# Kernel optimization log

Hardware: AMD Instinct MI355X
Metric: run time of the kernel (lower is better)

Reference implementation:

```python
import jax, jax.numpy as jnp
import numpy as np

MAX_N = 32        # mixture degree N
N_PTS = 16384     # number of scalar inputs
INIT_DECAY = 1.0


def setup_inputs() -> dict:
    key = jax.random.key(0)
    k1, _ = jax.random.split(key)
    # inputs assumed elementwise in [-1, 1]
    xs = jax.random.uniform(k1, (N_PTS,), dtype=jnp.float32, minval=-1.0, maxval=1.0)
    # learned logits param, init logits[n] = -n * init_decay (as in __init__)
    logits = -INIT_DECAY * jnp.arange(MAX_N + 1, dtype=jnp.float32)
    return {"xs": xs, "logits": logits}


def _psi(xs, logits, max_n):
    """psi(x) = concat_n sqrt(w_n) * phi_n(x); shape (P, 2*max_n+1).

    phi_0 = [1]; phi_n = [T_n(x), sqrt(1-x^2) * U_{n-1}(x)] for n>=1.
    Single linear-pass recurrence instead of per-degree recompute.
    """
    w = jax.nn.softmax(logits)          # (max_n+1,)
    sw = jnp.sqrt(w)
    xc = jnp.clip(xs, -1.0, 1.0)        # (P,)
    s = jnp.sqrt(jnp.clip(1.0 - xc * xc, 0.0))
    P = xs.shape[0]

    # T_0..T_max_n and U_0..U_max_n via one shared recurrence (fixed small loop)
    Ts = [jnp.ones_like(xc), xc]
    Us = [jnp.ones_like(xc), 2.0 * xc]
    for _ in range(2, max_n + 1):
        Ts.append(2.0 * xc * Ts[-1] - Ts[-2])
        Us.append(2.0 * xc * Us[-1] - Us[-2])
    T = jnp.stack(Ts, axis=-1)          # (P, max_n+1)
    U = jnp.stack(Us, axis=-1)          # (P, max_n+1)

    Tn = T[:, 1:]                       # T_1..T_N            (P, max_n)
    Un = U[:, :max_n]                   # U_0..U_{N-1}        (P, max_n)
    # interleave per degree: [T_n, s * U_{n-1}], weighted by sqrt(w_n)
    pair = jnp.stack([Tn, s[:, None] * Un], axis=-1)   # (P, max_n, 2)
    pair = pair * sw[1:][None, :, None]
    head = sw[0] * jnp.ones((P, 1), dtype=xs.dtype)    # sqrt(w_0) * phi_0
    return jnp.concatenate([head, pair.reshape(P, 2 * max_n)], axis=-1)


def reference(xs, logits):
    """gram(xs) = psi(xs) @ psi(xs)^T, shape (P, P)."""
    psi = _psi(xs, logits, MAX_N)       # (P, 2*MAX_N+1)
    return psi @ psi.T
```

## Files before the change

### kernel.cpp

```cpp
#include <hip/hip_runtime.h>
#include <hip/hip_bf16.h>
#include <math.h>

#define MAXN    32
#define NPTS    16384
#define RSTRIDE 64
#define BTA     64
#define BTB     128
#define NCHUNK  ((BTA + BTB) * RSTRIDE * 2 / 1024)
#define W0_OFF  (NPTS * RSTRIDE)

typedef __attribute__((ext_vector_type(8))) short         bf16x8;
typedef __attribute__((ext_vector_type(4))) float         f32x4;
typedef __attribute__((ext_vector_type(4))) unsigned int  u32x4;

__device__ inline ushort f2bf(float f) {
    union { float f; unsigned u; } v; v.f = f;
    unsigned u = v.u;
    u += 0x7FFFu + ((u >> 16) & 1u);
    return (ushort)(u >> 16);
}

__global__ __launch_bounds__(256) void psi_kernel(
    const float* __restrict__ xs, const float* __restrict__ logits,
    ushort* __restrict__ psi, float* __restrict__ w0scr)
{
    int pt = blockIdx.x * blockDim.x + threadIdx.x;
    if (pt >= NPTS) return;

    float x = xs[pt];
    x = fminf(1.0f, fmaxf(-1.0f, x));
    float s = sqrtf(fmaxf(0.0f, 1.0f - x * x));

    float m = -3.4e38f;
    #pragma unroll
    for (int n = 0; n <= MAXN; ++n) m = fmaxf(m, logits[n]);
    float sum = 0.0f;
    #pragma unroll
    for (int n = 0; n <= MAXN; ++n) sum += __expf(logits[n] - m);
    float inv = 1.0f / sum;

    if (pt == 0) w0scr[0] = __expf(logits[0] - m) * inv;

    ushort tmp[RSTRIDE];
    float Tm1 = 1.0f, T = x;
    float Um1 = 1.0f, U = 2.0f * x;
    float tx = 2.0f * x;
    #pragma unroll
    for (int n = 1; n <= MAXN; ++n) {
        float swn = sqrtf(__expf(logits[n] - m) * inv);
        tmp[2 * n - 2] = f2bf(swn * T);
        tmp[2 * n - 1] = f2bf(swn * (s * Um1));
        float Tn = tx * T - Tm1; Tm1 = T; T = Tn;
        float Un = tx * U - Um1; Um1 = U; U = Un;
    }

    u32x4* dst = (u32x4*)(psi + (size_t)pt * RSTRIDE);
    const u32x4* src = (const u32x4*)tmp;
    const int rx = pt & 7;
    #pragma unroll
    for (int j = 0; j < 8; ++j) dst[j ^ rx] = src[j];
}

__device__ inline void load_lds16(const void* g, void* l) {
    __builtin_amdgcn_global_load_lds(
        (const __attribute__((address_space(1))) unsigned*)g,
        (__attribute__((address_space(3))) unsigned*)l, 16, 0, 0);
}

__global__ __launch_bounds__(256, 5) void gram_kernel(
    const ushort* __restrict__ psi, const float* __restrict__ w0scr,
    float* __restrict__ out)
{
    __shared__ float ldsF[BTA * BTB];

    const int tid  = threadIdx.x;
    const int w    = tid >> 6;
    const int lane = tid & 63;
    const int bi   = blockIdx.y;
    const int bj   = blockIdx.x;

    const float w0 = w0scr[0];

    {
        const char* gA = (const char*)(psi + (size_t)bi * BTA * RSTRIDE);
        const char* gB = (const char*)(psi + (size_t)bj * BTB * RSTRIDE);
        char* lbase = (char*)ldsF;
        for (int q = w; q < NCHUNK; q += 4) {
            const char* src = (q < 8) ? (gA + q * 1024) : (gB + (q - 8) * 1024);
            load_lds16(src + lane * 16, lbase + q * 1024);
        }
    }
    __syncthreads();

    const int lr = lane & 15;
    const int lh = lane >> 4;
    const int cq = lh * 4;

    const char* aRow   = (const char*)ldsF + (w * 16 + lr) * 128;
    const char* bPanel = (const char*)ldsF + 8192;

    f32x4 acc[8];
    #pragma unroll
    for (int ct = 0; ct < 8; ++ct) acc[ct] = (f32x4){w0, w0, w0, w0};

    #pragma unroll
    for (int ks = 0; ks < 2; ++ks) {
        const int slot = (ks * 4 + lh);
        bf16x8 a = *(const bf16x8*)(aRow + ((slot ^ (lr & 7)) * 16));
        #pragma unroll
        for (int ct = 0; ct < 8; ++ct) {
            const char* bRow = bPanel + (ct * 16 + lr) * 128;
            bf16x8 b = *(const bf16x8*)(bRow + ((slot ^ (lr & 7)) * 16));
            acc[ct] = __builtin_amdgcn_mfma_f32_16x16x32_bf16(b, a, acc[ct], 0, 0, 0);
        }
    }

    __syncthreads();
    {
        const int row = w * 16 + lr;
        const int rxe = (row & 7) << 2;
        #pragma unroll
        for (int ct = 0; ct < 8; ++ct) {
            int col = (cq + ct * 16) ^ rxe;
            *(f32x4*)(ldsF + row * BTB + col) = acc[ct];
        }
    }
    __syncthreads();

    {
        const int rsub = tid >> 5;
        const int col  = (tid & 31) * 4;
        #pragma unroll
        for (int p = 0; p < 8; ++p) {
            int row  = p * 8 + rsub;
            int colr = col ^ ((row & 7) << 2);
            f32x4 v = *(const f32x4*)(ldsF + row * BTB + colr);
            float* dst = out + (size_t)(bi * BTA + row) * NPTS + (size_t)bj * BTB + col;
            *(f32x4*)dst = v;
        }
    }
}

extern "C" void kernel_launch(void* const* d_in, const int* in_sizes, int n_in,
                              void* d_out, int out_size, void* d_ws, size_t ws_size,
                              hipStream_t stream) {
    const float* xs     = (const float*)d_in[0];
    const float* logits = (const float*)d_in[1];
    float* out          = (float*)d_out;
    ushort* psi         = (ushort*)d_ws;
    float*  w0scr       = (float*)((char*)d_ws + (size_t)W0_OFF * 2);

    psi_kernel<<<NPTS / 256, 256, 0, stream>>>(xs, logits, psi, w0scr);

    dim3 grid(NPTS / BTB, NPTS / BTA);
    gram_kernel<<<grid, 256, 0, stream>>>(psi, w0scr, out);
}
```

Before: 200.4 us.

## Widen gram tile to 64x256, stage psi rows through LDS for coalesced stores

```diff
diff --git a/kernel.cpp b/kernel.cpp
--- a/kernel.cpp
+++ b/kernel.cpp
@@ -6,7 +6,7 @@
 #define NPTS    16384
 #define RSTRIDE 64
 #define BTA     64
-#define BTB     128
+#define BTB     256
 #define NCHUNK  ((BTA + BTB) * RSTRIDE * 2 / 1024)
 #define W0_OFF  (NPTS * RSTRIDE)
 
@@ -25,8 +25,10 @@
     const float* __restrict__ xs, const float* __restrict__ logits,
     ushort* __restrict__ psi, float* __restrict__ w0scr)
 {
-    int pt = blockIdx.x * blockDim.x + threadIdx.x;
-    if (pt >= NPTS) return;
+    __shared__ ushort srow[256 * RSTRIDE];
+
+    const int tid = threadIdx.x;
+    const int pt  = blockIdx.x * 256 + tid;
 
     float x = xs[pt];
     x = fminf(1.0f, fmaxf(-1.0f, x));
@@ -55,11 +57,21 @@
         float Un = tx * U - Um1; Um1 = U; U = Un;
     }
 
-    u32x4* dst = (u32x4*)(psi + (size_t)pt * RSTRIDE);
-    const u32x4* src = (const u32x4*)tmp;
-    const int rx = pt & 7;
-    #pragma unroll
-    for (int j = 0; j < 8; ++j) dst[j ^ rx] = src[j];
+    {
+        u32x4* lrow = (u32x4*)(srow + tid * RSTRIDE);
+        const u32x4* src = (const u32x4*)tmp;
+        const int rx = tid & 7;
+        #pragma unroll
+        for (int j = 0; j < 8; ++j) lrow[j ^ rx] = src[j];
+    }
+    __syncthreads();
+
+    {
+        const u32x4* ls = (const u32x4*)srow;
+        u32x4* gd = (u32x4*)(psi + (size_t)blockIdx.x * 256 * RSTRIDE);
+        #pragma unroll
+        for (int i = 0; i < 8; ++i) gd[i * 256 + tid] = ls[i * 256 + tid];
+    }
 }
 
 __device__ inline void load_lds16(const void* g, void* l) {
@@ -68,7 +80,7 @@
         (__attribute__((address_space(3))) unsigned*)l, 16, 0, 0);
 }
 
-__global__ __launch_bounds__(256, 5) void gram_kernel(
+__global__ __launch_bounds__(256) void gram_kernel(
     const ushort* __restrict__ psi, const float* __restrict__ w0scr,
     float* __restrict__ out)
 {
@@ -100,18 +112,17 @@
     const char* aRow   = (const char*)ldsF + (w * 16 + lr) * 128;
     const char* bPanel = (const char*)ldsF + 8192;
 
-    f32x4 acc[8];
+    f32x4 acc[16];
     #pragma unroll
-    for (int ct = 0; ct < 8; ++ct) acc[ct] = (f32x4){w0, w0, w0, w0};
+    for (int ct = 0; ct < 16; ++ct) acc[ct] = (f32x4){w0, w0, w0, w0};
 
     #pragma unroll
     for (int ks = 0; ks < 2; ++ks) {
-        const int slot = (ks * 4 + lh);
-        bf16x8 a = *(const bf16x8*)(aRow + ((slot ^ (lr & 7)) * 16));
+        const int sx = ((ks * 4 + lh) ^ (lr & 7)) * 16;
+        bf16x8 a = *(const bf16x8*)(aRow + sx);
         #pragma unroll
-        for (int ct = 0; ct < 8; ++ct) {
-            const char* bRow = bPanel + (ct * 16 + lr) * 128;
-            bf16x8 b = *(const bf16x8*)(bRow + ((slot ^ (lr & 7)) * 16));
+        for (int ct = 0; ct < 16; ++ct) {
+            bf16x8 b = *(const bf16x8*)(bPanel + (ct * 16 + lr) * 128 + sx);
             acc[ct] = __builtin_amdgcn_mfma_f32_16x16x32_bf16(b, a, acc[ct], 0, 0, 0);
         }
     }
@@ -121,7 +132,7 @@
         const int row = w * 16 + lr;
         const int rxe = (row & 7) << 2;
         #pragma unroll
-        for (int ct = 0; ct < 8; ++ct) {
+        for (int ct = 0; ct < 16; ++ct) {
             int col = (cq + ct * 16) ^ rxe;
             *(f32x4*)(ldsF + row * BTB + col) = acc[ct];
         }
@@ -129,14 +140,12 @@
     __syncthreads();
 
     {
-        const int rsub = tid >> 5;
-        const int col  = (tid & 31) * 4;
         #pragma unroll
-        for (int p = 0; p < 8; ++p) {
-            int row  = p * 8 + rsub;
-            int colr = col ^ ((row & 7) << 2);
+        for (int p = 0; p < 16; ++p) {
+            int row  = p * 4 + w;
+            int colr = (lane * 4) ^ ((row & 7) << 2);
             f32x4 v = *(const f32x4*)(ldsF + row * BTB + colr);
-            float* dst = out + (size_t)(bi * BTA + row) * NPTS + (size_t)bj * BTB + col;
+            float* dst = out + (size_t)(bi * BTA + row) * NPTS + (size_t)bj * BTB + lane * 4;
             *(f32x4*)dst = v;
         }
     }
```

Result: faster. 184.9 us (-7.7%).
